# Optimization experiments

Measured on AMD Instinct MI355X. Metric: run time of the kernel, lower is better.

## Reference

```python
import jax, jax.numpy as jnp
import numpy as np
from jax import lax

N, H, W, C = 4, 256, 256, 128
COUT = 128
BS_IN, BS_OUT, BSTR = 18, 16, 16  # gather block, conv-out block, block stride
N_ACTIVE = 512


def setup_inputs() -> dict:
    key = jax.random.key(0)
    ks = jax.random.split(key, 8)
    x = jax.random.normal(ks[0], (N, H, W, C), dtype=jnp.float32)
    w = jax.random.normal(ks[1], (3, 3, C, COUT), dtype=jnp.float32) * 0.05  # HWIO
    b = jax.random.normal(ks[2], (COUT,), dtype=jnp.float32) * 0.05
    gamma = jax.random.uniform(ks[3], (COUT,), dtype=jnp.float32, minval=0.5, maxval=1.5)
    beta = jax.random.normal(ks[4], (COUT,), dtype=jnp.float32) * 0.1
    mean = jax.random.normal(ks[5], (COUT,), dtype=jnp.float32) * 0.1
    var = jax.random.uniform(ks[6], (COUT,), dtype=jnp.float32, minval=0.5, maxval=1.5)
    # unique active block ids over the N x (H/16) x (W/16) grid -> disjoint scatter targets
    n_blocks = N * (H // BSTR) * (W // BSTR)
    active = jax.random.permutation(ks[7], n_blocks)[:N_ACTIVE].astype(jnp.int32)
    return {"x": x, "w": w, "b": b, "gamma": gamma, "beta": beta,
            "mean": mean, "var": var, "active": active}


def reference(x, w, b, gamma, beta, mean, var, active):
    n_, h_, w_, c_ = x.shape
    nby, nbx = h_ // BSTR, w_ // BSTR
    bn = active // (nby * nbx)
    rem = active % (nby * nbx)
    by = rem // nbx
    bx = rem % nbx

    # --- sparse_gather: overlapping BS_IN x BS_IN input blocks (zero-pad edges) ---
    pad = BS_IN - BS_OUT
    xp = jnp.pad(x, ((0, 0), (0, pad), (0, pad), (0, 0)))
    Hp, Wp = h_ + pad, w_ + pad
    d_in = jnp.arange(BS_IN, dtype=jnp.int32)
    hs = by[:, None] * BSTR + d_in[None, :]            # [Nb, 18]
    ws = bx[:, None] * BSTR + d_in[None, :]            # [Nb, 18]
    gidx = bn[:, None, None] * (Hp * Wp) + hs[:, :, None] * Wp + ws[:, None, :]
    p = xp.reshape(-1, c_)[gidx]                       # [Nb, 18, 18, C]

    # --- dense conv + BN(eval, eps=1e-3) + ReLU on gathered blocks ---
    q = lax.conv_general_dilated(p, w, window_strides=(1, 1), padding='VALID',
                                 dimension_numbers=('NHWC', 'HWIO', 'NHWC'))
    q = q + b
    q = (q - mean) * (gamma * lax.rsqrt(var + 1e-3)) + beta
    q = jax.nn.relu(q)                                 # [Nb, 16, 16, COUT]

    # --- sparse_scatter: write disjoint BS_OUT blocks back into a copy of x ---
    d_out = jnp.arange(BS_OUT, dtype=jnp.int32)
    hso = by[:, None] * BSTR + d_out[None, :]
    wso = bx[:, None] * BSTR + d_out[None, :]
    sidx = bn[:, None, None] * (h_ * w_) + hso[:, :, None] * w_ + wso[:, None, :]
    y = x.reshape(-1, c_).at[sidx.reshape(-1)].set(q.reshape(-1, q.shape[-1]))
    return y.reshape(n_, h_, w_, c_)
```

## Files before the change

### kernel.cpp

```cpp
#include <hip/hip_runtime.h>
#include <hip/hip_bf16.h>

#define H_ 256
#define W_ 256
#define C_ 128
#define NBPOS 1024
#define NACT 512

typedef __bf16 bf16x8 __attribute__((ext_vector_type(8)));
typedef float f32x4 __attribute__((ext_vector_type(4)));

#define SCALE_OFF 294912
#define SHIFT_OFF 295424
#define FLAGS_OFF 295936

__global__ void prep_w_kernel(const float* __restrict__ w, __bf16* __restrict__ wprep) {
  int o = blockIdx.x * 256 + threadIdx.x;
  int j = o & 7;
  int cout = (o >> 3) & 127;
  int k8 = (o >> 10) & 15;
  int tap = o >> 14;
  int cin = k8 * 8 + j;
  wprep[o] = (__bf16)w[((size_t)tap * 128 + cin) * 128 + cout];
}

__global__ void prep_misc_kernel(const float* __restrict__ b, const float* __restrict__ gamma,
                                 const float* __restrict__ beta, const float* __restrict__ mean,
                                 const float* __restrict__ var,
                                 float* __restrict__ scale, float* __restrict__ shift,
                                 int* __restrict__ flags) {
  int i = blockIdx.x * 256 + threadIdx.x;
  if (i < 128) {
    float s = gamma[i] / sqrtf(var[i] + 1e-3f);
    scale[i] = s;
    shift[i] = (b[i] - mean[i]) * s + beta[i];
  }
  if (i < NBPOS) flags[i] = 0;
}

__global__ void flags_set_kernel(const int* __restrict__ active, int* __restrict__ flags) {
  int i = blockIdx.x * 256 + threadIdx.x;
  if (i < NACT) flags[active[i]] = 1;
}

__global__ __launch_bounds__(256) void copy_kernel(const float* __restrict__ x,
                                                   const int* __restrict__ flags,
                                                   float* __restrict__ y) {
  int pb = blockIdx.x;
  if (flags[pb]) return;
  int bn = pb >> 8, by = (pb >> 4) & 15, bx = pb & 15;
  size_t base = (((size_t)bn * H_ + by * 16) * W_ + bx * 16) * C_;
  const float4* xs = (const float4*)x;
  float4* ys = (float4*)y;
  for (int i = threadIdx.x; i < 8192; i += 256) {
    int row = i >> 9;
    int rem = i & 511;
    size_t idx4 = (base + (size_t)row * (W_ * C_)) / 4 + rem;
    ys[idx4] = xs[idx4];
  }
}

__global__ __launch_bounds__(256, 2) void conv_kernel(
    const float* __restrict__ x, const __bf16* __restrict__ wprep,
    const float* __restrict__ scale, const float* __restrict__ shift,
    const int* __restrict__ active, float* __restrict__ y) {
  __shared__ unsigned char ldsA[324 * 128];
  __shared__ unsigned char ldsB[8192];

  const int tid = threadIdx.x;
  const int lane = tid & 63;
  const int wid = tid >> 6;
  const int aid = active[blockIdx.x];
  const int bn = aid >> 8;
  const int by = (aid >> 4) & 15;
  const int bx = aid & 15;
  const int h0 = by * 16, w0 = bx * 16;
  const float* xb = x + (size_t)bn * (H_ * W_ * C_);

  float sc[8], sh[8];
  {
    int col = lane & 15;
#pragma unroll
    for (int nb = 0; nb < 8; ++nb) {
      sc[nb] = scale[nb * 16 + col];
      sh[nb] = shift[nb * 16 + col];
    }
  }

  f32x4 acc[4][8];
  f32x4 zero = {0.f, 0.f, 0.f, 0.f};
#pragma unroll
  for (int i = 0; i < 4; ++i)
#pragma unroll
    for (int j = 0; j < 8; ++j) acc[i][j] = zero;

  const uint4* wp4 = (const uint4*)wprep;
  uint4 t0 = wp4[tid];
  uint4 t1 = wp4[256 + tid];

  const int koff = (lane >> 4) * 16;
  const int colb = (lane & 15) * 16;
  const int krow = (lane >> 4) * 2048;

  for (int half = 0; half < 2; ++half) {
    __syncthreads();
    for (int chunk = tid; chunk < 324 * 8; chunk += 256) {
      int s = chunk >> 3;
      int c8 = chunk & 7;
      int iy = s / 18;
      int ix = s - iy * 18;
      int hs = h0 + iy, wsp = w0 + ix;
      float4 f0 = make_float4(0.f, 0.f, 0.f, 0.f), f1 = make_float4(0.f, 0.f, 0.f, 0.f);
      if (hs < H_ && wsp < W_) {
        const float* p = xb + (size_t)(hs * W_ + wsp) * C_ + half * 64 + c8 * 8;
        f0 = *(const float4*)p;
        f1 = *(const float4*)(p + 4);
      }
      bf16x8 v;
      v[0] = (__bf16)f0.x; v[1] = (__bf16)f0.y; v[2] = (__bf16)f0.z; v[3] = (__bf16)f0.w;
      v[4] = (__bf16)f1.x; v[5] = (__bf16)f1.y; v[6] = (__bf16)f1.z; v[7] = (__bf16)f1.w;
      int lin = s * 128 + c8 * 16;
      *(bf16x8*)(&ldsA[lin ^ ((s & 7) << 4)]) = v;
    }
    for (int ks = 0; ks < 18; ++ks) {
      __syncthreads();
      ((uint4*)ldsB)[tid] = t0;
      ((uint4*)ldsB)[256 + tid] = t1;
      int u = half * 18 + ks + 1;
      if (u < 36) {
        int h2 = u / 18, k2 = u - (u / 18) * 18;
        int tile = (k2 >> 1) * 4 + h2 * 2 + (k2 & 1);
        t0 = wp4[tile * 512 + tid];
        t1 = wp4[tile * 512 + 256 + tid];
      }
      __syncthreads();

      int tap = ks >> 1, kch = ks & 1;
      int dyv = tap / 3, dxv = tap - dyv * 3;

      bf16x8 a[4];
#pragma unroll
      for (int mi = 0; mi < 4; ++mi) {
        int srow = (wid * 4 + mi + dyv) * 18 + dxv + (lane & 15);
        int lin = srow * 128 + kch * 64 + koff;
        a[mi] = *(const bf16x8*)(&ldsA[lin ^ ((srow & 7) << 4)]);
      }
      bf16x8 bfr[8];
#pragma unroll
      for (int nb = 0; nb < 8; ++nb)
        bfr[nb] = *(const bf16x8*)(&ldsB[krow + nb * 256 + colb]);
#pragma unroll
      for (int mi = 0; mi < 4; ++mi)
#pragma unroll
        for (int nb = 0; nb < 8; ++nb)
          acc[mi][nb] = __builtin_amdgcn_mfma_f32_16x16x32_bf16(a[mi], bfr[nb], acc[mi][nb], 0, 0, 0);
    }
  }

  const int colc = lane & 15;
  float* yb = y + (((size_t)bn * H_ + h0) * W_ + w0) * C_;
#pragma unroll
  for (int mi = 0; mi < 4; ++mi) {
    int oy = wid * 4 + mi;
#pragma unroll
    for (int r = 0; r < 4; ++r) {
      int ox = (lane >> 4) * 4 + r;
      float* yr = yb + ((size_t)oy * W_ + ox) * C_;
#pragma unroll
      for (int nb = 0; nb < 8; ++nb) {
        float v = acc[mi][nb][r] * sc[nb] + sh[nb];
        yr[nb * 16 + colc] = fmaxf(v, 0.f);
      }
    }
  }
}

extern "C" void kernel_launch(void* const* d_in, const int* in_sizes, int n_in,
                              void* d_out, int out_size, void* d_ws, size_t ws_size,
                              hipStream_t stream) {
  const float* x     = (const float*)d_in[0];
  const float* w     = (const float*)d_in[1];
  const float* b     = (const float*)d_in[2];
  const float* gamma = (const float*)d_in[3];
  const float* beta  = (const float*)d_in[4];
  const float* mean  = (const float*)d_in[5];
  const float* var   = (const float*)d_in[6];
  const int*   act   = (const int*)d_in[7];
  float* y = (float*)d_out;
  char* ws = (char*)d_ws;
  __bf16* wprep = (__bf16*)ws;
  float* scale = (float*)(ws + SCALE_OFF);
  float* shift = (float*)(ws + SHIFT_OFF);
  int* flags = (int*)(ws + FLAGS_OFF);

  prep_w_kernel<<<dim3(576), dim3(256), 0, stream>>>(w, wprep);
  prep_misc_kernel<<<dim3(4), dim3(256), 0, stream>>>(b, gamma, beta, mean, var, scale, shift, flags);
  flags_set_kernel<<<dim3(2), dim3(256), 0, stream>>>(act, flags);
  copy_kernel<<<dim3(NBPOS), dim3(256), 0, stream>>>(x, flags, y);
  conv_kernel<<<dim3(NACT), dim3(256), 0, stream>>>(x, wprep, scale, shift, act, y);
}
```

Measured before the change: 81.74 us.

## Fuse copy and conv into one grid, merge prep kernels, double-buffer weights

Merges the three small prep kernels into one launch plus a memset, and fuses the passthrough copy and the sparse conv into a single 1024-block kernel. Each block either copies its inactive tile or computes the conv for an active tile. The weight tile LDS is double-buffered so each K-step needs only one barrier instead of two. This cuts launch overhead and lets copy and conv work overlap on the GPU, at the cost of extra LDS per block and mixed block types in one grid.

```diff
diff --git a/kernel.cpp b/kernel.cpp
--- a/kernel.cpp
+++ b/kernel.cpp
@@ -14,67 +14,55 @@
 #define SHIFT_OFF 295424
 #define FLAGS_OFF 295936
 
-__global__ void prep_w_kernel(const float* __restrict__ w, __bf16* __restrict__ wprep) {
-  int o = blockIdx.x * 256 + threadIdx.x;
-  int j = o & 7;
-  int cout = (o >> 3) & 127;
-  int k8 = (o >> 10) & 15;
-  int tap = o >> 14;
-  int cin = k8 * 8 + j;
-  wprep[o] = (__bf16)w[((size_t)tap * 128 + cin) * 128 + cout];
-}
-
-__global__ void prep_misc_kernel(const float* __restrict__ b, const float* __restrict__ gamma,
-                                 const float* __restrict__ beta, const float* __restrict__ mean,
-                                 const float* __restrict__ var,
-                                 float* __restrict__ scale, float* __restrict__ shift,
-                                 int* __restrict__ flags) {
-  int i = blockIdx.x * 256 + threadIdx.x;
-  if (i < 128) {
-    float s = gamma[i] / sqrtf(var[i] + 1e-3f);
-    scale[i] = s;
-    shift[i] = (b[i] - mean[i]) * s + beta[i];
-  }
-  if (i < NBPOS) flags[i] = 0;
-}
-
-__global__ void flags_set_kernel(const int* __restrict__ active, int* __restrict__ flags) {
-  int i = blockIdx.x * 256 + threadIdx.x;
-  if (i < NACT) flags[active[i]] = 1;
-}
-
-__global__ __launch_bounds__(256) void copy_kernel(const float* __restrict__ x,
-                                                   const int* __restrict__ flags,
-                                                   float* __restrict__ y) {
-  int pb = blockIdx.x;
-  if (flags[pb]) return;
-  int bn = pb >> 8, by = (pb >> 4) & 15, bx = pb & 15;
-  size_t base = (((size_t)bn * H_ + by * 16) * W_ + bx * 16) * C_;
-  const float4* xs = (const float4*)x;
-  float4* ys = (float4*)y;
-  for (int i = threadIdx.x; i < 8192; i += 256) {
-    int row = i >> 9;
-    int rem = i & 511;
-    size_t idx4 = (base + (size_t)row * (W_ * C_)) / 4 + rem;
-    ys[idx4] = xs[idx4];
+__global__ void prep_kernel(const float* __restrict__ w, const float* __restrict__ b,
+                            const float* __restrict__ gamma, const float* __restrict__ beta,
+                            const float* __restrict__ mean, const float* __restrict__ var,
+                            const int* __restrict__ active,
+                            __bf16* __restrict__ wprep, float* __restrict__ scale,
+                            float* __restrict__ shift, int* __restrict__ flags) {
+  int blk = blockIdx.x, tid = threadIdx.x;
+  if (blk < 576) {
+    int o = blk * 256 + tid;
+    int j = o & 7, cout = (o >> 3) & 127, k8 = (o >> 10) & 15, tap = o >> 14;
+    wprep[o] = (__bf16)w[((size_t)tap * 128 + k8 * 8 + j) * 128 + cout];
+  } else {
+    if (tid < 128) {
+      float s = gamma[tid] * rsqrtf(var[tid] + 1e-3f);
+      scale[tid] = s;
+      shift[tid] = (b[tid] - mean[tid]) * s + beta[tid];
+    }
+    for (int i = tid; i < NACT; i += 256) flags[active[i]] = 1;
   }
 }
 
-__global__ __launch_bounds__(256, 2) void conv_kernel(
+__global__ __launch_bounds__(256, 2) void fused_kernel(
     const float* __restrict__ x, const __bf16* __restrict__ wprep,
     const float* __restrict__ scale, const float* __restrict__ shift,
-    const int* __restrict__ active, float* __restrict__ y) {
+    const int* __restrict__ flags, float* __restrict__ y) {
   __shared__ unsigned char ldsA[324 * 128];
-  __shared__ unsigned char ldsB[8192];
+  __shared__ unsigned char ldsB[2][8192];
 
+  const int pb = blockIdx.x;
   const int tid = threadIdx.x;
+  const int bn = pb >> 8, by = (pb >> 4) & 15, bx = pb & 15;
+  const int h0 = by * 16, w0 = bx * 16;
+
+  if (!flags[pb]) {
+    size_t base4 = ((((size_t)bn * H_ + h0) * W_ + w0) * C_) >> 2;
+    const float4* __restrict__ xs = (const float4*)x;
+    float4* __restrict__ ys = (float4*)y;
+#pragma unroll 8
+    for (int i = 0; i < 32; ++i) {
+      int lin = (i << 8) + tid;
+      int row = lin >> 9, rem = lin & 511;
+      size_t idx4 = base4 + (size_t)row * (W_ * C_ / 4) + rem;
+      ys[idx4] = xs[idx4];
+    }
+    return;
+  }
+
   const int lane = tid & 63;
   const int wid = tid >> 6;
-  const int aid = active[blockIdx.x];
-  const int bn = aid >> 8;
-  const int by = (aid >> 4) & 15;
-  const int bx = aid & 15;
-  const int h0 = by * 16, w0 = bx * 16;
   const float* xb = x + (size_t)bn * (H_ * W_ * C_);
 
   float sc[8], sh[8];
@@ -95,22 +83,19 @@
     for (int j = 0; j < 8; ++j) acc[i][j] = zero;
 
   const uint4* wp4 = (const uint4*)wprep;
-  uint4 t0 = wp4[tid];
-  uint4 t1 = wp4[256 + tid];
-
-  const int koff = (lane >> 4) * 16;
-  const int colb = (lane & 15) * 16;
-  const int krow = (lane >> 4) * 2048;
-
-  for (int half = 0; half < 2; ++half) {
-    __syncthreads();
+  uint4 t0, t1;
+  auto load_t = [&](int u) {
+    int ks = u % 18, h = u / 18;
+    int tile = ((ks >> 1) << 2) + (h << 1) + (ks & 1);
+    t0 = wp4[tile * 512 + tid];
+    t1 = wp4[tile * 512 + 256 + tid];
+  };
+  auto stage = [&](int half) {
     for (int chunk = tid; chunk < 324 * 8; chunk += 256) {
-      int s = chunk >> 3;
-      int c8 = chunk & 7;
-      int iy = s / 18;
-      int ix = s - iy * 18;
+      int s = chunk >> 3, c8 = chunk & 7;
+      int iy = s / 18, ix = s - iy * 18;
       int hs = h0 + iy, wsp = w0 + ix;
-      float4 f0 = make_float4(0.f, 0.f, 0.f, 0.f), f1 = make_float4(0.f, 0.f, 0.f, 0.f);
+      float4 f0 = make_float4(0.f, 0.f, 0.f, 0.f), f1 = f0;
       if (hs < H_ && wsp < W_) {
         const float* p = xb + (size_t)(hs * W_ + wsp) * C_ + half * 64 + c8 * 8;
         f0 = *(const float4*)p;
@@ -122,38 +107,51 @@
       int lin = s * 128 + c8 * 16;
       *(bf16x8*)(&ldsA[lin ^ ((s & 7) << 4)]) = v;
     }
-    for (int ks = 0; ks < 18; ++ks) {
-      __syncthreads();
-      ((uint4*)ldsB)[tid] = t0;
-      ((uint4*)ldsB)[256 + tid] = t1;
-      int u = half * 18 + ks + 1;
-      if (u < 36) {
-        int h2 = u / 18, k2 = u - (u / 18) * 18;
-        int tile = (k2 >> 1) * 4 + h2 * 2 + (k2 & 1);
-        t0 = wp4[tile * 512 + tid];
-        t1 = wp4[tile * 512 + 256 + tid];
-      }
-      __syncthreads();
+  };
 
-      int tap = ks >> 1, kch = ks & 1;
-      int dyv = tap / 3, dxv = tap - dyv * 3;
+  load_t(0);
+  stage(0);
+  ((uint4*)ldsB[0])[tid] = t0;
+  ((uint4*)ldsB[0])[256 + tid] = t1;
+  load_t(1);
+  __syncthreads();
 
-      bf16x8 a[4];
+  const int koff = (lane >> 4) * 16;
+  const int colb = (lane & 15) * 16;
+  const int krow = (lane >> 4) * 2048;
+
+  for (int u = 0; u < 36; ++u) {
+    int cur = u & 1;
+    if (u < 35) {
+      ((uint4*)ldsB[cur ^ 1])[tid] = t0;
+      ((uint4*)ldsB[cur ^ 1])[256 + tid] = t1;
+      if (u < 34) load_t(u + 2);
+    }
+    int ks = u % 18;
+    int tap = ks >> 1, kch = ks & 1;
+    int dyv = tap / 3, dxv = tap - dyv * 3;
+
+    bf16x8 a[4];
 #pragma unroll
-      for (int mi = 0; mi < 4; ++mi) {
-        int srow = (wid * 4 + mi + dyv) * 18 + dxv + (lane & 15);
-        int lin = srow * 128 + kch * 64 + koff;
-        a[mi] = *(const bf16x8*)(&ldsA[lin ^ ((srow & 7) << 4)]);
-      }
-      bf16x8 bfr[8];
+    for (int mi = 0; mi < 4; ++mi) {
+      int srow = (wid * 4 + mi + dyv) * 18 + dxv + (lane & 15);
+      int lin = srow * 128 + kch * 64 + koff;
+      a[mi] = *(const bf16x8*)(&ldsA[lin ^ ((srow & 7) << 4)]);
+    }
+    bf16x8 bfr[8];
+#pragma unroll
+    for (int nb = 0; nb < 8; ++nb)
+      bfr[nb] = *(const bf16x8*)(&ldsB[cur][krow + nb * 256 + colb]);
+#pragma unroll
+    for (int mi = 0; mi < 4; ++mi)
 #pragma unroll
       for (int nb = 0; nb < 8; ++nb)
-        bfr[nb] = *(const bf16x8*)(&ldsB[krow + nb * 256 + colb]);
-#pragma unroll
-      for (int mi = 0; mi < 4; ++mi)
-#pragma unroll
-        for (int nb = 0; nb < 8; ++nb)
-          acc[mi][nb] = __builtin_amdgcn_mfma_f32_16x16x32_bf16(a[mi], bfr[nb], acc[mi][nb], 0, 0, 0);
+        acc[mi][nb] = __builtin_amdgcn_mfma_f32_16x16x32_bf16(a[mi], bfr[nb], acc[mi][nb], 0, 0, 0);
+
+    __syncthreads();
+    if (u == 17) {
+      stage(1);
+      __syncthreads();
     }
   }
 
@@ -193,9 +191,8 @@
   float* shift = (float*)(ws + SHIFT_OFF);
   int* flags = (int*)(ws + FLAGS_OFF);
 
-  prep_w_kernel<<<dim3(576), dim3(256), 0, stream>>>(w, wprep);
-  prep_misc_kernel<<<dim3(4), dim3(256), 0, stream>>>(b, gamma, beta, mean, var, scale, shift, flags);
-  flags_set_kernel<<<dim3(2), dim3(256), 0, stream>>>(act, flags);
-  copy_kernel<<<dim3(NBPOS), dim3(256), 0, stream>>>(x, flags, y);
-  conv_kernel<<<dim3(NACT), dim3(256), 0, stream>>>(x, wprep, scale, shift, act, y);
+  hipMemsetAsync(flags, 0, NBPOS * sizeof(int), stream);
+  prep_kernel<<<dim3(577), dim3(256), 0, stream>>>(w, b, gamma, beta, mean, var, act,
+                                                   wprep, scale, shift, flags);
+  fused_kernel<<<dim3(NBPOS), dim3(256), 0, stream>>>(x, wprep, scale, shift, flags, y);
 }
```

Result: slower. 92.14 us (+12.7%).
